# Kernel tuning notes

Hardware: AMD Instinct MI355X
Metric: run time of the kernel (lower is better)

## Reference

```python
import jax, jax.numpy as jnp
import numpy as np

B, S, D = 2, 2048, 2048
HQ, HKV, HD, HDV = 32, 8, 64, 64
QPK = HQ // HKV
EPS = 1e-5


def setup_inputs() -> dict:
    key = jax.random.key(0)
    ks = jax.random.split(key, 10)
    s = lambda fan_in: 1.0 / np.sqrt(fan_in)
    return {
        'x': jax.random.normal(ks[0], (B, S, D), dtype=jnp.float32),
        'ln_g': jnp.ones((D,), jnp.float32),
        'ln_b': jnp.zeros((D,), jnp.float32),
        'Wq': jax.random.uniform(ks[1], (D, HQ * HD), jnp.float32, -s(D), s(D)),
        'bq': jax.random.uniform(ks[2], (HQ * HD,), jnp.float32, -s(D), s(D)),
        'Wk': jax.random.uniform(ks[3], (D, HKV * HD), jnp.float32, -s(D), s(D)),
        'bk': jax.random.uniform(ks[4], (HKV * HD,), jnp.float32, -s(D), s(D)),
        'Wv': jax.random.uniform(ks[5], (D, HKV * HDV), jnp.float32, -s(D), s(D)),
        'bv': jax.random.uniform(ks[6], (HKV * HDV,), jnp.float32, -s(D), s(D)),
        'Wo': jax.random.uniform(ks[7], (HQ * HDV, D), jnp.float32, -s(HQ * HDV), s(HQ * HDV)),
        'bo': jax.random.uniform(ks[8], (D,), jnp.float32, -s(HQ * HDV), s(HQ * HDV)),
    }


def reference(x, ln_g, ln_b, Wq, bq, Wk, bk, Wv, bv, Wo, bo):
    # LayerNorm
    mu = jnp.mean(x, axis=-1, keepdims=True)
    var = jnp.mean(jnp.square(x - mu), axis=-1, keepdims=True)
    xn = (x - mu) * jax.lax.rsqrt(var + EPS) * ln_g + ln_b

    q = (xn @ Wq + bq).reshape(B, S, HKV, QPK, HD) * (1.0 / np.sqrt(HD))
    k = (xn @ Wk + bk).reshape(B, S, HKV, HD)
    v = (xn @ Wv + bv).reshape(B, S, HKV, HDV)

    # scores: (b, t=query, T=key, h, q_per_kv)
    scores = jnp.einsum('bthqd,bThd->btThq', q, k)
    # causal mask: -inf where T > t (upper triangle above diagonal)
    mask = jnp.triu(jnp.full((S, S), -jnp.inf, dtype=scores.dtype), 1)
    scores = scores + mask[None, :, :, None, None]
    # NOTE: source softmaxes over dim=-4, i.e. the QUERY axis t -> axis=1 here
    scores = jax.nn.softmax(scores, axis=1)
    out = jnp.einsum('btThq,bThd->bthqd', scores, v)
    out = out.reshape(B, S, HQ * HDV)
    return out @ Wo + bo
```

## Files before the change

kernel.cpp:

```cpp
#include <hip/hip_runtime.h>

#define Bb  2
#define Ss  2048
#define Dd  2048
#define HKV 8
#define QPK 4
#define HD  64
#define MR  (Bb * Ss)
#define NQ  2048
#define NKV 512

#define LOG2E 1.4426950408889634f

typedef unsigned short u16;
typedef unsigned int u32;
typedef __attribute__((ext_vector_type(8))) short s16x8;
typedef __attribute__((ext_vector_type(4))) float f32x4;

__device__ __forceinline__ u16 f2bf(float f) {
  unsigned u = __float_as_uint(f);
  u += 0x7fffu + ((u >> 16) & 1u);
  return (u16)(u >> 16);
}

__device__ __forceinline__ void gload16(const u16* g, u16* l) {
  __builtin_amdgcn_global_load_lds(
      (const __attribute__((address_space(1))) unsigned int*)g,
      (__attribute__((address_space(3))) unsigned int*)l, 16, 0, 0);
}

__device__ __forceinline__ u32 cvtpk_bf16(float a, float b) {
  u32 r;
  asm volatile("v_cvt_pk_bf16_f32 %0, %1, %2" : "=v"(r) : "v"(a), "v"(b));
  return r;
}

__global__ __launch_bounds__(256) void ln_kernel(
    const float* __restrict__ x, const float* __restrict__ g,
    const float* __restrict__ be, u16* __restrict__ xn)
{
  int row = blockIdx.x;
  int tid = threadIdx.x;
  const float4* xr = (const float4*)(x + (size_t)row * Dd);
  float4 a = xr[tid];
  float4 b4 = xr[tid + 256];
  float s  = a.x + a.y + a.z + a.w + b4.x + b4.y + b4.z + b4.w;
  float ss = a.x*a.x + a.y*a.y + a.z*a.z + a.w*a.w
           + b4.x*b4.x + b4.y*b4.y + b4.z*b4.z + b4.w*b4.w;
  #pragma unroll
  for (int off = 32; off > 0; off >>= 1) {
    s  += __shfl_down(s, off);
    ss += __shfl_down(ss, off);
  }
  __shared__ float red[8];
  int lane = tid & 63, w = tid >> 6;
  if (lane == 0) { red[w] = s; red[4 + w] = ss; }
  __syncthreads();
  s  = red[0] + red[1] + red[2] + red[3];
  ss = red[4] + red[5] + red[6] + red[7];
  float mu = s * (1.0f / Dd);
  float rs = rsqrtf(ss * (1.0f / Dd) - mu * mu + 1e-5f);

  u16* xo = xn + (size_t)row * Dd;
  const float4* gv4 = (const float4*)g;
  const float4* bv4 = (const float4*)be;
  #pragma unroll
  for (int p = 0; p < 2; ++p) {
    int idx = tid + p * 256;
    float4 xv = (p == 0) ? a : b4;
    float4 gg = gv4[idx], bb = bv4[idx];
    ushort4 pk;
    pk.x = f2bf((xv.x - mu) * rs * gg.x + bb.x);
    pk.y = f2bf((xv.y - mu) * rs * gg.y + bb.y);
    pk.z = f2bf((xv.z - mu) * rs * gg.z + bb.z);
    pk.w = f2bf((xv.w - mu) * rs * gg.w + bb.w);
    *(ushort4*)(xo + idx * 4) = pk;
  }
}

__global__ __launch_bounds__(256) void transpose_cast(
    const float* __restrict__ W, u16* __restrict__ WT, int K, int N)
{
  __shared__ float tile[32][33];
  int tx = threadIdx.x & 31, ty = threadIdx.x >> 5;
  int n0 = blockIdx.x * 32, k0 = blockIdx.y * 32;
  #pragma unroll
  for (int i = 0; i < 4; ++i)
    tile[ty + 8 * i][tx] = W[(size_t)(k0 + ty + 8 * i) * N + n0 + tx];
  __syncthreads();
  #pragma unroll
  for (int i = 0; i < 4; ++i)
    WT[(size_t)(n0 + ty + 8 * i) * K + k0 + tx] = f2bf(tile[tx][ty + 8 * i]);
}

__global__ __launch_bounds__(256) void transpose_v(
    const u16* __restrict__ vb, u16* __restrict__ vT)
{
  __shared__ u16 tile[32][33];
  int tx = threadIdx.x & 31, ty = threadIdx.x >> 5;
  int c0 = blockIdx.x * 32;
  int r0 = blockIdx.y * 32;
  #pragma unroll
  for (int i = 0; i < 4; ++i)
    tile[ty + 8 * i][tx] = vb[(size_t)(r0 + ty + 8 * i) * NKV + c0 + tx];
  __syncthreads();
  int b = r0 >> 11, t = r0 & 2047;
  #pragma unroll
  for (int i = 0; i < 4; ++i)
    vT[((size_t)(b * NKV + c0 + ty + 8 * i)) * Ss + t + tx] = tile[tx][ty + 8 * i];
}

__device__ __forceinline__ void gemm_core128(
    const u16* __restrict__ A, const u16* __restrict__ BT, int K,
    int brow128, int bcol128, u16* __restrict__ As, u16* __restrict__ Bs,
    f32x4 (&acc)[4][4])
{
  int tid  = threadIdx.x;
  int lane = tid & 63, wave = tid >> 6;
  int wm = (wave >> 1) * 64, wn = (wave & 1) * 64;
  int m16 = lane & 15, quad = lane >> 4;
  int srow = lane >> 3;
  int scol = (lane & 7) * 8;
  const u16* Ag = A  + (size_t)(brow128 + wave * 32 + srow) * K + scol;
  const u16* Bg = BT + (size_t)(bcol128 + wave * 32 + srow) * K + scol;
  u16* Asw = As + (size_t)(wave * 32) * 64;
  u16* Bsw = Bs + (size_t)(wave * 32) * 64;

  for (int k0 = 0; k0 < K; k0 += 64) {
    __syncthreads();
    #pragma unroll
    for (int i = 0; i < 4; ++i) {
      gload16(Ag + (size_t)(i * 8) * K + k0, Asw + i * 512);
      gload16(Bg + (size_t)(i * 8) * K + k0, Bsw + i * 512);
    }
    __syncthreads();
    s16x8 af[4][2], bf[4][2];
    #pragma unroll
    for (int i = 0; i < 4; ++i) {
      af[i][0] = *(const s16x8*)&As[(size_t)(wm + i * 16 + m16) * 64 + quad * 8];
      af[i][1] = *(const s16x8*)&As[(size_t)(wm + i * 16 + m16) * 64 + 32 + quad * 8];
      bf[i][0] = *(const s16x8*)&Bs[(size_t)(wn + i * 16 + m16) * 64 + quad * 8];
      bf[i][1] = *(const s16x8*)&Bs[(size_t)(wn + i * 16 + m16) * 64 + 32 + quad * 8];
    }
    #pragma unroll
    for (int i = 0; i < 4; ++i)
      #pragma unroll
      for (int j = 0; j < 4; ++j) {
        acc[i][j] = __builtin_amdgcn_mfma_f32_16x16x32_bf16(af[i][0], bf[j][0], acc[i][j], 0, 0, 0);
        acc[i][j] = __builtin_amdgcn_mfma_f32_16x16x32_bf16(af[i][1], bf[j][1], acc[i][j], 0, 0, 0);
      }
  }
}

template<bool BF16OUT>
__global__ __launch_bounds__(256) void gemm_bt2(
    const u16* __restrict__ A, const u16* __restrict__ BT,
    const float* __restrict__ bias, void* __restrict__ Cv,
    int N, int K, float scale)
{
  __shared__ u16 As[128 * 64];
  __shared__ u16 Bs[128 * 64];
  f32x4 acc[4][4] = {};
  gemm_core128(A, BT, K, blockIdx.y * 128, blockIdx.x * 128, As, Bs, acc);

  int lane = threadIdx.x & 63, wave = threadIdx.x >> 6;
  int wm = (wave >> 1) * 64, wn = (wave & 1) * 64;
  int m16 = lane & 15, quad = lane >> 4;
  #pragma unroll
  for (int i = 0; i < 4; ++i) {
    #pragma unroll
    for (int j = 0; j < 4; ++j) {
      int col = blockIdx.x * 128 + wn + j * 16 + m16;
      float bcol = bias[col];
      #pragma unroll
      for (int r = 0; r < 4; ++r) {
        int rowg = blockIdx.y * 128 + wm + i * 16 + quad * 4 + r;
        float val = (acc[i][j][r] + bcol) * scale;
        if constexpr (BF16OUT)
          ((u16*)Cv)[(size_t)rowg * N + col] = f2bf(val);
        else
          ((float*)Cv)[(size_t)rowg * N + col] = val;
      }
    }
  }
}

__global__ __launch_bounds__(256) void gemm_qkv(
    const u16* __restrict__ A, const u16* __restrict__ BT,
    const float* __restrict__ bq, const float* __restrict__ bk,
    const float* __restrict__ bv,
    u16* __restrict__ qb, u16* __restrict__ kb, u16* __restrict__ vb)
{
  __shared__ u16 As[128 * 64];
  __shared__ u16 Bs[128 * 64];
  f32x4 acc[4][4] = {};
  gemm_core128(A, BT, Dd, blockIdx.y * 128, blockIdx.x * 128, As, Bs, acc);

  u16* outp; const float* bp; int ldo, colbase; float scale;
  if (blockIdx.x < 16)      { outp = qb; bp = bq; ldo = NQ;  colbase = blockIdx.x * 128;        scale = 0.125f * LOG2E; }
  else if (blockIdx.x < 20) { outp = kb; bp = bk; ldo = NKV; colbase = (blockIdx.x - 16) * 128; scale = 1.0f; }
  else                      { outp = vb; bp = bv; ldo = NKV; colbase = (blockIdx.x - 20) * 128; scale = 1.0f; }

  int lane = threadIdx.x & 63, wave = threadIdx.x >> 6;
  int wm = (wave >> 1) * 64, wn = (wave & 1) * 64;
  int m16 = lane & 15, quad = lane >> 4;
  #pragma unroll
  for (int i = 0; i < 4; ++i) {
    #pragma unroll
    for (int j = 0; j < 4; ++j) {
      int col = colbase + wn + j * 16 + m16;
      float bcol = bp[col];
      #pragma unroll
      for (int r = 0; r < 4; ++r) {
        int rowg = blockIdx.y * 128 + wm + i * 16 + quad * 4 + r;
        outp[(size_t)rowg * ldo + col] = f2bf((acc[i][j][r] + bcol) * scale);
      }
    }
  }
}

__global__ __launch_bounds__(256) void pass_a_mfma(
    const u16* __restrict__ qb, const u16* __restrict__ kb,
    float* __restrict__ cst)
{
  __shared__ u16 Qs[64 * 64];
  int combo = blockIdx.x;
  int qk = combo & 3, bh = combo >> 2;
  int b = bh >> 3, h = bh & 7;
  int g = blockIdx.y;
  int tid = threadIdx.x;
  int lane = tid & 63, wave = tid >> 6;
  int m16 = lane & 15, quad = lane >> 4;
  int T0w = g * 128 + wave * 32;

  const u16* kbase = kb + (size_t)b * Ss * NKV + h * HD;
  const u16* qbase = qb + (size_t)b * Ss * NQ + (h * QPK + qk) * HD;

  s16x8 kf[2][2];
  #pragma unroll
  for (int jg = 0; jg < 2; ++jg)
    #pragma unroll
    for (int dc = 0; dc < 2; ++dc)
      kf[jg][dc] = *(const s16x8*)(kbase + (size_t)(T0w + jg * 16 + m16) * NKV + dc * 32 + quad * 8);

  float ms[2] = {-1e30f, -1e30f};
  float ls[2] = {0.f, 0.f};
  int srow  = (wave << 3) + (lane >> 3);
  int slot0 = (lane & 7) ^ (lane >> 3);
  u16* QsW = Qs + (size_t)(wave * 8) * 64;
  int sl0 = quad ^ (m16 & 7);
  int sl1 = (quad | 4) ^ (m16 & 7);
  int tDiag = T0w & ~63;

  for (int t0 = g * 128; t0 < Ss; t0 += 64) {
    __syncthreads();
    gload16(qbase + (size_t)(t0 + srow) * NQ + slot0 * 8, QsW);
    gload16(qbase + (size_t)(t0 + srow + 32) * NQ + slot0 * 8, QsW + 32 * 64);
    __syncthreads();
    if (t0 + 63 < T0w) continue;

    s16x8 af[4][2];
    #pragma unroll
    for (int i = 0; i < 4; ++i) {
      af[i][0] = *(const s16x8*)&Qs[(i * 16 + m16) * 64 + sl0 * 8];
      af[i][1] = *(const s16x8*)&Qs[(i * 16 + m16) * 64 + sl1 * 8];
    }
    f32x4 acc[4][2];
    #pragma unroll
    for (int i = 0; i < 4; ++i)
      #pragma unroll
      for (int jg = 0; jg < 2; ++jg) {
        f32x4 z = {};
        z = __builtin_amdgcn_mfma_f32_16x16x32_bf16(af[i][0], kf[jg][0], z, 0, 0, 0);
        acc[i][jg] = __builtin_amdgcn_mfma_f32_16x16x32_bf16(af[i][1], kf[jg][1], z, 0, 0, 0);
      }
    if (t0 == tDiag) {
      #pragma unroll
      for (int i = 0; i < 4; ++i)
        #pragma unroll
        for (int jg = 0; jg < 2; ++jg) {
          int tg = t0 + i * 16 + quad * 4;
          int Tg = T0w + jg * 16 + m16;
          #pragma unroll
          for (int r = 0; r < 4; ++r)
            if (tg + r < Tg) acc[i][jg][r] = -3e38f;
        }
    }
    #pragma unroll
    for (int jg = 0; jg < 2; ++jg) {
      float bm = -3e38f;
      #pragma unroll
      for (int i = 0; i < 4; ++i)
        #pragma unroll
        for (int r = 0; r < 4; ++r) bm = fmaxf(bm, acc[i][jg][r]);
      float mn = fmaxf(ms[jg], bm);
      float se = 0.f;
      #pragma unroll
      for (int i = 0; i < 4; ++i)
        #pragma unroll
        for (int r = 0; r < 4; ++r) se += exp2f(acc[i][jg][r] - mn);
      ls[jg] = ls[jg] * exp2f(ms[jg] - mn) + se;
      ms[jg] = mn;
    }
  }
  #pragma unroll
  for (int jg = 0; jg < 2; ++jg) {
    float m = ms[jg], l = ls[jg];
    #pragma unroll
    for (int off = 16; off <= 32; off <<= 1) {
      float mo = __shfl_xor(m, off);
      float lo = __shfl_xor(l, off);
      float mn = fmaxf(m, mo);
      l = l * exp2f(m - mn) + lo * exp2f(mo - mn);
      m = mn;
    }
    if (quad == 0)
      cst[(size_t)(bh * QPK + qk) * Ss + T0w + jg * 16 + m16] = m + __log2f(l);
  }
}

__global__ __launch_bounds__(256) void pass_b_mfma(
    const u16* __restrict__ qb, const u16* __restrict__ kb,
    const u16* __restrict__ vT, const float* __restrict__ cst,
    u16* __restrict__ attn)
{
  __shared__ u16 Ks[64 * 64];
  __shared__ u16 Vs[64 * 64];
  int combo = blockIdx.x;
  int qk = combo & 3, bh = combo >> 2;
  int b = bh >> 3, h = bh & 7;
  int g = 31 - blockIdx.y;
  int tid = threadIdx.x;
  int lane = tid & 63, wave = tid >> 6;
  int m16 = lane & 15, quad = lane >> 4;
  int trow = g * 64 + wave * 16;

  const u16* qbase = qb + (size_t)b * Ss * NQ + (h * QPK + qk) * HD;
  const u16* kbase = kb + (size_t)b * Ss * NKV + h * HD;
  const u16* vbase = vT + (size_t)(bh * 64) * Ss;
  const float* cbase = cst + (size_t)(bh * QPK + qk) * Ss;

  s16x8 qf[2];
  #pragma unroll
  for (int dc = 0; dc < 2; ++dc)
    qf[dc] = *(const s16x8*)(qbase + (size_t)(trow + m16) * NQ + dc * 32 + quad * 8);

  f32x4 oacc[4] = {};
  int srow  = (wave << 3) + (lane >> 3);
  int slot0 = (lane & 7) ^ (lane >> 3);
  u16* KsW = Ks + (size_t)(wave * 8) * 64;
  u16* VsW = Vs + (size_t)(wave * 8) * 64;
  int sl0 = quad ^ (m16 & 7);
  int sl1 = (quad | 4) ^ (m16 & 7);
  int Tend = g * 64;

  for (int T0 = 0; T0 <= Tend; T0 += 64) {
    __syncthreads();
    gload16(kbase + (size_t)(T0 + srow) * NKV + slot0 * 8, KsW);
    gload16(kbase + (size_t)(T0 + srow + 32) * NKV + slot0 * 8, KsW + 32 * 64);
    gload16(vbase + (size_t)srow * Ss + T0 + slot0 * 8, VsW);
    gload16(vbase + (size_t)(srow + 32) * Ss + T0 + slot0 * 8, VsW + 32 * 64);
    __syncthreads();
    bool diag = (T0 == Tend);
    #pragma unroll
    for (int tc = 0; tc < 2; ++tc) {
      u32 A[2], Bw[2];
      #pragma unroll
      for (int ii = 0; ii < 2; ++ii) {
        int i = tc * 2 + ii;
        s16x8 k0 = *(const s16x8*)&Ks[(i * 16 + m16) * 64 + sl0 * 8];
        s16x8 k1 = *(const s16x8*)&Ks[(i * 16 + m16) * 64 + sl1 * 8];
        f32x4 z = {};
        z = __builtin_amdgcn_mfma_f32_16x16x32_bf16(k0, qf[0], z, 0, 0, 0);
        z = __builtin_amdgcn_mfma_f32_16x16x32_bf16(k1, qf[1], z, 0, 0, 0);
        float4 cc = *(const float4*)(cbase + T0 + i * 16 + quad * 4);
        float w0 = exp2f(z[0] - cc.x);
        float w1 = exp2f(z[1] - cc.y);
        float w2 = exp2f(z[2] - cc.z);
        float w3 = exp2f(z[3] - cc.w);
        if (diag) {
          int t  = trow + m16;
          int Tg = T0 + i * 16 + quad * 4;
          if (Tg + 0 > t) w0 = 0.f;
          if (Tg + 1 > t) w1 = 0.f;
          if (Tg + 2 > t) w2 = 0.f;
          if (Tg + 3 > t) w3 = 0.f;
        }
        A[ii]  = cvtpk_bf16(w0, w1);
        Bw[ii] = cvtpk_bf16(w2, w3);
      }
      asm volatile("v_permlane32_swap_b32 %0, %1" : "+v"(A[0]),  "+v"(A[1]));
      asm volatile("v_permlane16_swap_b32 %0, %1" : "+v"(A[0]),  "+v"(A[1]));
      asm volatile("v_permlane32_swap_b32 %0, %1" : "+v"(Bw[0]), "+v"(Bw[1]));
      asm volatile("v_permlane16_swap_b32 %0, %1" : "+v"(Bw[0]), "+v"(Bw[1]));
      union { uint4 u; s16x8 v; } pu;
      pu.u.x = A[0]; pu.u.y = Bw[0]; pu.u.z = A[1]; pu.u.w = Bw[1];
      s16x8 pa = pu.v;
      #pragma unroll
      for (int dj = 0; dj < 4; ++dj) {
        int vsl = (quad | (tc << 2)) ^ (m16 & 7);
        s16x8 vf = *(const s16x8*)&Vs[(dj * 16 + m16) * 64 + vsl * 8];
        oacc[dj] = __builtin_amdgcn_mfma_f32_16x16x32_bf16(pa, vf, oacc[dj], 0, 0, 0);
      }
    }
  }
  u16* abase = attn + (size_t)b * Ss * NQ + (h * QPK + qk) * HD;
  #pragma unroll
  for (int dj = 0; dj < 4; ++dj)
    #pragma unroll
    for (int r = 0; r < 4; ++r)
      abase[(size_t)(trow + quad * 4 + r) * NQ + dj * 16 + m16] = f2bf(oacc[dj][r]);
}

extern "C" void kernel_launch(void* const* d_in, const int* in_sizes, int n_in,
                              void* d_out, int out_size, void* d_ws, size_t ws_size,
                              hipStream_t stream)
{
  (void)in_sizes; (void)n_in; (void)out_size; (void)ws_size;
  const float* x   = (const float*)d_in[0];
  const float* lng = (const float*)d_in[1];
  const float* lnb = (const float*)d_in[2];
  const float* Wq  = (const float*)d_in[3];
  const float* bq  = (const float*)d_in[4];
  const float* Wk  = (const float*)d_in[5];
  const float* bk  = (const float*)d_in[6];
  const float* Wv  = (const float*)d_in[7];
  const float* bv  = (const float*)d_in[8];
  const float* Wo  = (const float*)d_in[9];
  const float* bo  = (const float*)d_in[10];
  float* out = (float*)d_out;

  char* ws = (char*)d_ws;
  size_t off = 0;
  auto take = [&](size_t bytes) -> char* {
    char* p = ws + off;
    off += (bytes + 255) & ~(size_t)255;
    return p;
  };
  u16*    xnb   = (u16*)take((size_t)MR * Dd * 2);
  u16*    wqkvT = (u16*)take((size_t)(NQ + 2 * NKV) * Dd * 2);
  u16*    woT   = (u16*)take((size_t)Dd * NQ * 2);
  u16*    qbB   = (u16*)take((size_t)MR * NQ * 2);
  u16*    kbB   = (u16*)take((size_t)MR * NKV * 2);
  u16*    vbB   = (u16*)take((size_t)MR * NKV * 2);
  u16*    vTb   = (u16*)take((size_t)MR * NKV * 2);
  float*  cst   = (float*)take((size_t)Bb * HKV * QPK * Ss * 4);
  u16*    attnb = (u16*)take((size_t)MR * NQ * 2);

  ln_kernel<<<MR, 256, 0, stream>>>(x, lng, lnb, xnb);
  transpose_cast<<<dim3(NQ / 32, Dd / 32), 256, 0, stream>>>(Wq, wqkvT, Dd, NQ);
  transpose_cast<<<dim3(NKV / 32, Dd / 32), 256, 0, stream>>>(Wk, wqkvT + (size_t)NQ * Dd, Dd, NKV);
  transpose_cast<<<dim3(NKV / 32, Dd / 32), 256, 0, stream>>>(Wv, wqkvT + (size_t)(NQ + NKV) * Dd, Dd, NKV);
  transpose_cast<<<dim3(NQ / 32, Dd / 32), 256, 0, stream>>>(Wo, woT, Dd, NQ);

  gemm_qkv<<<dim3((NQ + 2 * NKV) / 128, MR / 128), 256, 0, stream>>>(
      xnb, wqkvT, bq, bk, bv, qbB, kbB, vbB);
  transpose_v<<<dim3(NKV / 32, MR / 32), 256, 0, stream>>>(vbB, vTb);

  pass_a_mfma<<<dim3(64, 16), 256, 0, stream>>>(qbB, kbB, cst);
  pass_b_mfma<<<dim3(64, 32), 256, 0, stream>>>(qbB, kbB, vTb, cst, attnb);

  gemm_bt2<false><<<dim3(Dd / 128, MR / 128), 256, 0, stream>>>(
      attnb, woT, bo, out, Dd, NQ, 1.0f);
}
```

Measured before the change: 397.8 us.

## Replace GEMMs with 256x256 double-buffered 8-wave swizzled MFMA kernel

Replaces the simple 128x128 single-buffered GEMM core used by the QKV and output projections with a 256x256-tile, 512-thread kernel. It double-buffers LDS with direct global-to-LDS loads issued ahead of the MFMA phases, XOR-swizzles the LDS layout to avoid bank conflicts, raises wave priority around MFMA bursts, and remaps workgroup IDs for L2 locality. The aim is to hide global-load latency and raise reuse per loaded tile. In exchange it uses 128KB of LDS and a large accumulator per thread, and launches only 192 and 128 workgroups, which may underfill the GPU.

Measured after the change: 385.6 us. 3.1% less time.

```diff
diff --git a/kernel.cpp b/kernel.cpp
--- a/kernel.cpp
+++ b/kernel.cpp
@@ -34,6 +34,10 @@
   asm volatile("v_cvt_pk_bf16_f32 %0, %1, %2" : "=v"(r) : "v"(a), "v"(b));
   return r;
 }
+
+#define BAR()    asm volatile("s_barrier" ::: "memory")
+#define WAITV4() asm volatile("s_waitcnt vmcnt(4)" ::: "memory")
+#define WAITV0() asm volatile("s_waitcnt vmcnt(0)" ::: "memory")
 
 __global__ __launch_bounds__(256) void ln_kernel(
     const float* __restrict__ x, const float* __restrict__ g,
@@ -110,112 +114,167 @@
     vT[((size_t)(b * NKV + c0 + ty + 8 * i)) * Ss + t + tx] = tile[tx][ty + 8 * i];
 }
 
-__device__ __forceinline__ void gemm_core128(
+__device__ __forceinline__ void gemm8_core(
     const u16* __restrict__ A, const u16* __restrict__ BT, int K,
-    int brow128, int bcol128, u16* __restrict__ As, u16* __restrict__ Bs,
-    f32x4 (&acc)[4][4])
-{
-  int tid  = threadIdx.x;
-  int lane = tid & 63, wave = tid >> 6;
-  int wm = (wave >> 1) * 64, wn = (wave & 1) * 64;
+    int brow, int bcol, u16* __restrict__ As, u16* __restrict__ Bs,
+    f32x4 (&acc)[8][4])
+{
+  const int tid  = threadIdx.x;
+  const int lane = tid & 63;
+  const int wave = tid >> 6;
+  const int wr = wave >> 2, wc = wave & 3;
+  const int m16 = lane & 15, quad = lane >> 4;
+  const int NT = K >> 6;
+
+  const int r0 = tid >> 3;
+  const int sg = (tid & 7) ^ (r0 & 7);
+  const u16* Asrc = A  + (size_t)(brow + r0) * K + sg * 8;
+  const u16* Bsrc = BT + (size_t)(bcol + r0) * K + sg * 8;
+  u16* AsW = As + wave * 512;
+  u16* BsW = Bs + wave * 512;
+  const size_t a64 = (size_t)64 * K;
+
+  const int sl0 = (quad ^ (m16 & 7)) * 8;
+  const int sl1 = ((quad | 4) ^ (m16 & 7)) * 8;
+  const u16* Afr = As + wr * 8192 + m16 * 64;
+  const u16* Bfr = Bs + (wc >> 1) * 8192 + ((wc & 1) * 64 + m16) * 64;
+
+  #pragma unroll
+  for (int h = 0; h < 2; ++h) {
+    gload16(Asrc + (size_t)(h * 128) * K, AsW + h * 8192);
+    gload16(Asrc + (size_t)(h * 128) * K + a64, AsW + h * 8192 + 4096);
+    gload16(Bsrc + (size_t)(h * 128) * K, BsW + h * 8192);
+    gload16(Bsrc + (size_t)(h * 128) * K + a64, BsW + h * 8192 + 4096);
+  }
+  #pragma unroll
+  for (int h = 0; h < 2; ++h) {
+    gload16(Bsrc + (size_t)(h * 128) * K + 64, BsW + 16384 + h * 8192);
+    gload16(Bsrc + (size_t)(h * 128) * K + a64 + 64, BsW + 16384 + h * 8192 + 4096);
+  }
+  WAITV4();
+  BAR();
+
+  for (int t = 0; t < NT; ++t) {
+    const int bi = t & 1;
+    const u16* Abuf = Afr + bi * 16384;
+    const u16* Bbuf = Bfr + bi * 16384;
+    s16x8 bfr[4][2];
+    #pragma unroll
+    for (int ph = 0; ph < 4; ++ph) {
+      s16x8 a0k0 = *(const s16x8*)(Abuf + (ph * 2 + 0) * 1024 + sl0);
+      s16x8 a0k1 = *(const s16x8*)(Abuf + (ph * 2 + 0) * 1024 + sl1);
+      s16x8 a1k0 = *(const s16x8*)(Abuf + (ph * 2 + 1) * 1024 + sl0);
+      s16x8 a1k1 = *(const s16x8*)(Abuf + (ph * 2 + 1) * 1024 + sl1);
+      if (ph == 0) {
+        #pragma unroll
+        for (int nj = 0; nj < 4; ++nj) {
+          bfr[nj][0] = *(const s16x8*)(Bbuf + nj * 1024 + sl0);
+          bfr[nj][1] = *(const s16x8*)(Bbuf + nj * 1024 + sl1);
+        }
+      }
+      if (ph < 2) {
+        if (t + 1 < NT) {
+          const u16* g = Asrc + (size_t)(ph * 128) * K + (t + 1) * 64;
+          u16* l = AsW + (bi ^ 1) * 16384 + ph * 8192;
+          gload16(g, l);
+          gload16(g + a64, l + 4096);
+        }
+      } else {
+        if (t + 2 < NT) {
+          const u16* g = Bsrc + (size_t)((ph - 2) * 128) * K + (t + 2) * 64;
+          u16* l = BsW + bi * 16384 + (ph - 2) * 8192;
+          gload16(g, l);
+          gload16(g + a64, l + 4096);
+        }
+      }
+      BAR();
+      __builtin_amdgcn_s_setprio(1);
+      #pragma unroll
+      for (int nj = 0; nj < 4; ++nj) {
+        acc[ph*2+0][nj] = __builtin_amdgcn_mfma_f32_16x16x32_bf16(a0k0, bfr[nj][0], acc[ph*2+0][nj], 0, 0, 0);
+        acc[ph*2+0][nj] = __builtin_amdgcn_mfma_f32_16x16x32_bf16(a0k1, bfr[nj][1], acc[ph*2+0][nj], 0, 0, 0);
+        acc[ph*2+1][nj] = __builtin_amdgcn_mfma_f32_16x16x32_bf16(a1k0, bfr[nj][0], acc[ph*2+1][nj], 0, 0, 0);
+        acc[ph*2+1][nj] = __builtin_amdgcn_mfma_f32_16x16x32_bf16(a1k1, bfr[nj][1], acc[ph*2+1][nj], 0, 0, 0);
+      }
+      __builtin_amdgcn_s_setprio(0);
+      if (ph == 3) {
+        if (t + 2 < NT) WAITV4(); else WAITV0();
+      }
+      BAR();
+    }
+  }
+}
+
+__global__ __launch_bounds__(512) void gemm8_bt(
+    const u16* __restrict__ A, const u16* __restrict__ BT,
+    const float* __restrict__ bias, float* __restrict__ C, int N, int K)
+{
+  __shared__ u16 As[32768];
+  __shared__ u16 Bs[32768];
+  int nbx = N >> 8;
+  int id  = blockIdx.y * nbx + blockIdx.x;
+  int nwg = gridDim.x * gridDim.y;
+  int swz = (id & 7) * (nwg >> 3) + (id >> 3);
+  int bx = swz % nbx, by = swz / nbx;
+
+  f32x4 acc[8][4] = {};
+  gemm8_core(A, BT, K, by * 256, bx * 256, As, Bs, acc);
+
+  int lane = threadIdx.x & 63, wave = threadIdx.x >> 6;
+  int wr = wave >> 2, wc = wave & 3;
   int m16 = lane & 15, quad = lane >> 4;
-  int srow = lane >> 3;
-  int scol = (lane & 7) * 8;
-  const u16* Ag = A  + (size_t)(brow128 + wave * 32 + srow) * K + scol;
-  const u16* Bg = BT + (size_t)(bcol128 + wave * 32 + srow) * K + scol;
-  u16* Asw = As + (size_t)(wave * 32) * 64;
-  u16* Bsw = Bs + (size_t)(wave * 32) * 64;
-
-  for (int k0 = 0; k0 < K; k0 += 64) {
-    __syncthreads();
-    #pragma unroll
-    for (int i = 0; i < 4; ++i) {
-      gload16(Ag + (size_t)(i * 8) * K + k0, Asw + i * 512);
-      gload16(Bg + (size_t)(i * 8) * K + k0, Bsw + i * 512);
-    }
-    __syncthreads();
-    s16x8 af[4][2], bf[4][2];
-    #pragma unroll
-    for (int i = 0; i < 4; ++i) {
-      af[i][0] = *(const s16x8*)&As[(size_t)(wm + i * 16 + m16) * 64 + quad * 8];
-      af[i][1] = *(const s16x8*)&As[(size_t)(wm + i * 16 + m16) * 64 + 32 + quad * 8];
-      bf[i][0] = *(const s16x8*)&Bs[(size_t)(wn + i * 16 + m16) * 64 + quad * 8];
-      bf[i][1] = *(const s16x8*)&Bs[(size_t)(wn + i * 16 + m16) * 64 + 32 + quad * 8];
-    }
-    #pragma unroll
-    for (int i = 0; i < 4; ++i)
-      #pragma unroll
-      for (int j = 0; j < 4; ++j) {
-        acc[i][j] = __builtin_amdgcn_mfma_f32_16x16x32_bf16(af[i][0], bf[j][0], acc[i][j], 0, 0, 0);
-        acc[i][j] = __builtin_amdgcn_mfma_f32_16x16x32_bf16(af[i][1], bf[j][1], acc[i][j], 0, 0, 0);
-      }
-  }
-}
-
-template<bool BF16OUT>
-__global__ __launch_bounds__(256) void gemm_bt2(
-    const u16* __restrict__ A, const u16* __restrict__ BT,
-    const float* __restrict__ bias, void* __restrict__ Cv,
-    int N, int K, float scale)
-{
-  __shared__ u16 As[128 * 64];
-  __shared__ u16 Bs[128 * 64];
-  f32x4 acc[4][4] = {};
-  gemm_core128(A, BT, K, blockIdx.y * 128, blockIdx.x * 128, As, Bs, acc);
-
-  int lane = threadIdx.x & 63, wave = threadIdx.x >> 6;
-  int wm = (wave >> 1) * 64, wn = (wave & 1) * 64;
-  int m16 = lane & 15, quad = lane >> 4;
-  #pragma unroll
-  for (int i = 0; i < 4; ++i) {
-    #pragma unroll
-    for (int j = 0; j < 4; ++j) {
-      int col = blockIdx.x * 128 + wn + j * 16 + m16;
-      float bcol = bias[col];
-      #pragma unroll
-      for (int r = 0; r < 4; ++r) {
-        int rowg = blockIdx.y * 128 + wm + i * 16 + quad * 4 + r;
-        float val = (acc[i][j][r] + bcol) * scale;
-        if constexpr (BF16OUT)
-          ((u16*)Cv)[(size_t)rowg * N + col] = f2bf(val);
-        else
-          ((float*)Cv)[(size_t)rowg * N + col] = val;
-      }
-    }
-  }
-}
-
-__global__ __launch_bounds__(256) void gemm_qkv(
+  int colb = bx * 256 + (wc >> 1) * 128 + (wc & 1) * 64;
+  #pragma unroll
+  for (int nj = 0; nj < 4; ++nj) {
+    int col = colb + nj * 16 + m16;
+    float bc = bias[col];
+    #pragma unroll
+    for (int mi = 0; mi < 8; ++mi)
+      #pragma unroll
+      for (int rr = 0; rr < 4; ++rr) {
+        int row = by * 256 + wr * 128 + mi * 16 + quad * 4 + rr;
+        C[(size_t)row * N + col] = acc[mi][nj][rr] + bc;
+      }
+  }
+}
+
+__global__ __launch_bounds__(512) void gemm8_qkv(
     const u16* __restrict__ A, const u16* __restrict__ BT,
     const float* __restrict__ bq, const float* __restrict__ bk,
     const float* __restrict__ bv,
     u16* __restrict__ qb, u16* __restrict__ kb, u16* __restrict__ vb)
 {
-  __shared__ u16 As[128 * 64];
-  __shared__ u16 Bs[128 * 64];
-  f32x4 acc[4][4] = {};
-  gemm_core128(A, BT, Dd, blockIdx.y * 128, blockIdx.x * 128, As, Bs, acc);
-
-  u16* outp; const float* bp; int ldo, colbase; float scale;
-  if (blockIdx.x < 16)      { outp = qb; bp = bq; ldo = NQ;  colbase = blockIdx.x * 128;        scale = 0.125f * LOG2E; }
-  else if (blockIdx.x < 20) { outp = kb; bp = bk; ldo = NKV; colbase = (blockIdx.x - 16) * 128; scale = 1.0f; }
-  else                      { outp = vb; bp = bv; ldo = NKV; colbase = (blockIdx.x - 20) * 128; scale = 1.0f; }
+  __shared__ u16 As[32768];
+  __shared__ u16 Bs[32768];
+  int nbx = 12;
+  int id  = blockIdx.y * nbx + blockIdx.x;
+  int nwg = 192;
+  int swz = (id & 7) * (nwg >> 3) + (id >> 3);
+  int bx = swz % nbx, by = swz / nbx;
+
+  f32x4 acc[8][4] = {};
+  gemm8_core(A, BT, Dd, by * 256, bx * 256, As, Bs, acc);
+
+  u16* outp; const float* bp; int ldo, cb; float scale;
+  if (bx < 8)       { outp = qb; bp = bq; ldo = NQ;  cb = bx * 256;        scale = 0.125f * LOG2E; }
+  else if (bx < 10) { outp = kb; bp = bk; ldo = NKV; cb = (bx - 8) * 256;  scale = 1.0f; }
+  else              { outp = vb; bp = bv; ldo = NKV; cb = (bx - 10) * 256; scale = 1.0f; }
 
   int lane = threadIdx.x & 63, wave = threadIdx.x >> 6;
-  int wm = (wave >> 1) * 64, wn = (wave & 1) * 64;
+  int wr = wave >> 2, wc = wave & 3;
   int m16 = lane & 15, quad = lane >> 4;
-  #pragma unroll
-  for (int i = 0; i < 4; ++i) {
-    #pragma unroll
-    for (int j = 0; j < 4; ++j) {
-      int col = colbase + wn + j * 16 + m16;
-      float bcol = bp[col];
-      #pragma unroll
-      for (int r = 0; r < 4; ++r) {
-        int rowg = blockIdx.y * 128 + wm + i * 16 + quad * 4 + r;
-        outp[(size_t)rowg * ldo + col] = f2bf((acc[i][j][r] + bcol) * scale);
-      }
-    }
+  int colb = cb + (wc >> 1) * 128 + (wc & 1) * 64;
+  #pragma unroll
+  for (int nj = 0; nj < 4; ++nj) {
+    int col = colb + nj * 16 + m16;
+    float bc = bp[col];
+    #pragma unroll
+    for (int mi = 0; mi < 8; ++mi)
+      #pragma unroll
+      for (int rr = 0; rr < 4; ++rr) {
+        int row = by * 256 + wr * 128 + mi * 16 + quad * 4 + rr;
+        outp[(size_t)row * ldo + col] = f2bf((acc[mi][nj][rr] + bc) * scale);
+      }
   }
 }
 
@@ -453,13 +512,11 @@
   transpose_cast<<<dim3(NKV / 32, Dd / 32), 256, 0, stream>>>(Wv, wqkvT + (size_t)(NQ + NKV) * Dd, Dd, NKV);
   transpose_cast<<<dim3(NQ / 32, Dd / 32), 256, 0, stream>>>(Wo, woT, Dd, NQ);
 
-  gemm_qkv<<<dim3((NQ + 2 * NKV) / 128, MR / 128), 256, 0, stream>>>(
-      xnb, wqkvT, bq, bk, bv, qbB, kbB, vbB);
+  gemm8_qkv<<<dim3(12, 16), 512, 0, stream>>>(xnb, wqkvT, bq, bk, bv, qbB, kbB, vbB);
   transpose_v<<<dim3(NKV / 32, MR / 32), 256, 0, stream>>>(vbB, vTb);
 
   pass_a_mfma<<<dim3(64, 16), 256, 0, stream>>>(qbB, kbB, cst);
   pass_b_mfma<<<dim3(64, 32), 256, 0, stream>>>(qbB, kbB, vTb, cst, attnb);
 
-  gemm_bt2<false><<<dim3(Dd / 128, MR / 128), 256, 0, stream>>>(
-      attnb, woT, bo, out, Dd, NQ, 1.0f);
-}
+  gemm8_bt<<<dim3(8, 16), 512, 0, stream>>>(attnb, woT, bo, out, Dd, NQ);
+}
```
